# Kernel optimization log

Measured on AMD Instinct MI355X. Metric: run time of the kernel, lower is better.

## Reference

```python
import jax, jax.numpy as jnp
import numpy as np

B, C, CI, H, W = 16, 256, 128, 64, 64


def setup_inputs() -> dict:
    key = jax.random.key(0)
    k1, k2, k3, k4, k5, k6 = jax.random.split(key, 6)
    x_gallery = jax.random.normal(k1, (B, C, H, W), dtype=jnp.float32)
    x_query = jax.random.normal(k2, (B, C, H, W), dtype=jnp.float32)
    # 1x1 conv weights (kernel_size=1 -> equivalent to per-pixel linear map)
    s = 1.0 / np.sqrt(C)
    theta_w = jax.random.uniform(k3, (CI, C), jnp.float32, -s, s)
    theta_b = jax.random.uniform(k4, (CI,), jnp.float32, -s, s)
    phi_w = jax.random.uniform(k5, (CI, C), jnp.float32, -s, s)
    phi_b = jax.random.uniform(k6, (CI,), jnp.float32, -s, s)
    return {"x_gallery": x_gallery, "x_query": x_query,
            "theta_w": theta_w, "theta_b": theta_b,
            "phi_w": phi_w, "phi_b": phi_b}


def reference(x_gallery, x_query, theta_w, theta_b, phi_w, phi_b):
    b, c, h, w = x_gallery.shape
    # 1x1 convs == channel-mixing einsum
    theta_x = jnp.einsum('bchw,oc->bohw', x_gallery, theta_w) + theta_b[None, :, None, None]
    phi_x = jnp.einsum('bchw,oc->bohw', x_query, phi_w) + phi_b[None, :, None, None]
    t = theta_x.reshape(b, theta_x.shape[1], -1)   # [B, CI, HW]
    p = phi_x.reshape(b, phi_x.shape[1], -1)       # [B, CI, H'W']
    n = p.shape[-1]
    # f[b, i, j] = <theta[:, i], phi[:, j]> / N   (norm == 'size')
    f = jnp.einsum('bci,bcj->bij', t, p) / n       # [B, HW, H'W']
    f = jnp.max(f, axis=2)                         # row-wise max (non-softmax attention)
    f = f.reshape(b, 1, h, w)
    return jax.nn.sigmoid(f)                       # message == 'attention_map'
```

## Files before the change

kernel.cpp:

```cpp
#include <hip/hip_runtime.h>
#include <hip/hip_bf16.h>

#define B_   16
#define CIN  256
#define CO   128
#define HW   4096

typedef __attribute__((ext_vector_type(8))) short short8;
typedef __attribute__((ext_vector_type(4))) float f32x4;

__device__ __forceinline__ short f32_to_bf16_rne(float f) {
    union { float f; unsigned u; } v; v.f = f;
    unsigned u = v.u;
    u += 0x7fffu + ((u >> 16) & 1u);
    return (short)(u >> 16);
}

__global__ __launch_bounds__(256) void wconv_kernel(
    const float* __restrict__ tw, const float* __restrict__ pw,
    short* __restrict__ wbf)
{
    const int idx = blockIdx.x * 256 + threadIdx.x;
    const float v = (idx < CO * CIN) ? tw[idx] : pw[idx - CO * CIN];
    wbf[idx] = f32_to_bf16_rne(v);
}

__global__ __launch_bounds__(256, 3) void proj_kernel(
    const float* __restrict__ xg, const float* __restrict__ xq,
    const float* __restrict__ tb, const float* __restrict__ pb,
    const short* __restrict__ wbf,
    short* __restrict__ tT, short* __restrict__ pT)
{
    const int n     = blockIdx.x;
    const int xcd   = n & 7;
    const int q     = n >> 3;
    const int b     = xcd + 8 * (q & 1);
    const int r2    = q >> 1;
    const int which = r2 & 1;
    const int itile = r2 >> 1;

    const float* x    = which ? xq : xg;
    const float* bias = which ? pb : tb;
    const short* wb   = wbf + which * CO * CIN;
    short*       out  = which ? pT : tT;

    const int i0   = itile * 64;
    const int tid  = threadIdx.x;
    const int lane = tid & 63;
    const int wv   = tid >> 6;
    const int nrow = lane & 15;
    const int quad = lane >> 4;

    const int col4 = tid & 15;
    const int rp   = tid >> 4;

    __shared__ short xT[2][64][72];

    f32x4 acc[4][2] = {};

    float bias_v[2];
    bias_v[0] = bias[wv * 32 + 0  + nrow];
    bias_v[1] = bias[wv * 32 + 16 + nrow];

    short8 wfrag[4][2][2];
    #pragma unroll
    for (int c4 = 0; c4 < 4; c4++)
        #pragma unroll
        for (int ks = 0; ks < 2; ks++)
            #pragma unroll
            for (int nt = 0; nt < 2; nt++)
                wfrag[c4][ks][nt] = *(const short8*)(
                    wb + (wv * 32 + nt * 16 + nrow) * CIN + c4 * 64 + ks * 32 + quad * 8);

    const float* xb = x + (long)b * CIN * HW + i0;

    float4 cva[2], cvb[2];

    auto load_chunk = [&](int cc) {
        #pragma unroll
        for (int rr = 0; rr < 2; rr++) {
            const int row = rr * 32 + rp * 2;
            cva[rr] = *(const float4*)(xb + (long)(cc + row)     * HW + col4 * 4);
            cvb[rr] = *(const float4*)(xb + (long)(cc + row + 1) * HW + col4 * 4);
        }
    };
    auto store_chunk = [&](int buf) {
        #pragma unroll
        for (int rr = 0; rr < 2; rr++) {
            const int row = rr * 32 + rp * 2;
            const float* pa  = (const float*)&cva[rr];
            const float* pb2 = (const float*)&cvb[rr];
            #pragma unroll
            for (int k = 0; k < 4; k++) {
                const unsigned lo = (unsigned short)f32_to_bf16_rne(pa[k]);
                const unsigned hi = (unsigned short)f32_to_bf16_rne(pb2[k]);
                *(unsigned*)&xT[buf][col4 * 4 + k][row] = lo | (hi << 16);
            }
        }
    };
    auto mfma_chunk = [&](int c4, int buf) {
        #pragma unroll
        for (int ks = 0; ks < 2; ks++)
            #pragma unroll
            for (int mt = 0; mt < 4; mt++) {
                const short8 a = *(const short8*)&xT[buf][mt * 16 + nrow][ks * 32 + quad * 8];
                acc[mt][0] = __builtin_amdgcn_mfma_f32_16x16x32_bf16(a, wfrag[c4][ks][0], acc[mt][0], 0, 0, 0);
                acc[mt][1] = __builtin_amdgcn_mfma_f32_16x16x32_bf16(a, wfrag[c4][ks][1], acc[mt][1], 0, 0, 0);
            }
    };

    load_chunk(0);
    store_chunk(0);
    #pragma unroll
    for (int c4 = 0; c4 < 4; c4++) {
        __syncthreads();
        if (c4 < 3) load_chunk(c4 * 64 + 64);
        mfma_chunk(c4, c4 & 1);
        if (c4 < 3) store_chunk((c4 + 1) & 1);
    }

    #pragma unroll
    for (int mt = 0; mt < 4; mt++)
        #pragma unroll
        for (int nt = 0; nt < 2; nt++) {
            const int co = wv * 32 + nt * 16 + nrow;
            #pragma unroll
            for (int r = 0; r < 4; r++) {
                const int il = mt * 16 + quad * 4 + r;
                out[((long)b * HW + i0 + il) * CO + co] =
                    f32_to_bf16_rne(acc[mt][nt][r] + bias_v[nt]);
            }
        }
}

__global__ __launch_bounds__(256, 1) void maxgemm_kernel(
    const short* __restrict__ tT, const short* __restrict__ pT,
    float* __restrict__ pmax)
{
    const int n     = blockIdx.x;
    const int b     = (n & 7) + 8 * ((n >> 3) & 1);
    const int mm    = n >> 4;
    const int itile = mm & 7;
    const int jhalf = mm >> 3;
    const int i0    = itile * 512;
    const int j0    = jhalf * 2048;
    const int tid   = threadIdx.x;
    const int lane  = tid & 63;
    const int wv    = tid >> 6;
    const int nrow  = lane & 15;
    const int quad  = lane >> 4;

    __shared__ short bT[2][64][128];

    short8 afrag[8][4];
    {
        const short* ta = tT + ((long)b * HW + i0 + wv * 128) * CO;
        #pragma unroll
        for (int mt = 0; mt < 8; mt++)
            #pragma unroll
            for (int ks = 0; ks < 4; ks++)
                afrag[mt][ks] = *(const short8*)(ta + (mt * 16 + nrow) * CO + ks * 32 + quad * 8);
    }

    const short* pb2 = pT + (long)b * HW * CO + (long)j0 * CO;
    const int sc8 = tid & 15;
    const int sj0 = tid >> 4;

    short8 sreg[4];
    auto stage_load = [&](int jt) {
        const short* src = pb2 + (long)jt * 64 * CO;
        #pragma unroll
        for (int r = 0; r < 4; r++)
            sreg[r] = *(const short8*)(src + (sj0 + r * 16) * CO + sc8 * 8);
    };
    auto stage_write = [&](int buf) {
        #pragma unroll
        for (int r = 0; r < 4; r++) {
            const int j  = sj0 + r * 16;
            const int c8 = sc8 ^ (j & 7);
            *(short8*)&bT[buf][j][c8 * 8] = sreg[r];
        }
    };

    f32x4 vmax[8];
    #pragma unroll
    for (int mt = 0; mt < 8; mt++)
        vmax[mt] = (f32x4){-1e30f, -1e30f, -1e30f, -1e30f};

    const f32x4 kz = {0.f, 0.f, 0.f, 0.f};

    auto compute = [&](int buf) {
        #pragma unroll
        for (int np = 0; np < 2; np++) {
            short8 bf0[4], bf1[4];
            const int ja = np * 32 + nrow;
            const int jb = ja + 16;
            #pragma unroll
            for (int ks = 0; ks < 4; ks++) {
                bf0[ks] = *(const short8*)&bT[buf][ja][(((ks * 4 + quad) ^ (ja & 7)) * 8)];
                bf1[ks] = *(const short8*)&bT[buf][jb][(((ks * 4 + quad) ^ (jb & 7)) * 8)];
            }
            #pragma unroll
            for (int mt = 0; mt < 8; mt++) {
                f32x4 a0 = __builtin_amdgcn_mfma_f32_16x16x32_bf16(afrag[mt][0], bf0[0], kz, 0, 0, 0);
                f32x4 a1 = __builtin_amdgcn_mfma_f32_16x16x32_bf16(afrag[mt][0], bf1[0], kz, 0, 0, 0);
                #pragma unroll
                for (int ks = 1; ks < 4; ks++) {
                    a0 = __builtin_amdgcn_mfma_f32_16x16x32_bf16(afrag[mt][ks], bf0[ks], a0, 0, 0, 0);
                    a1 = __builtin_amdgcn_mfma_f32_16x16x32_bf16(afrag[mt][ks], bf1[ks], a1, 0, 0, 0);
                }
                #pragma unroll
                for (int r = 0; r < 4; r++)
                    vmax[mt][r] = fmaxf(fmaxf(a0[r], a1[r]), vmax[mt][r]);
            }
        }
    };

    stage_load(0);
    stage_write(0);
    for (int jt = 0; jt < 32; jt++) {
        __syncthreads();
        if (jt < 31) stage_load(jt + 1);
        compute(jt & 1);
        if (jt < 31) stage_write((jt + 1) & 1);
    }

    #pragma unroll
    for (int mt = 0; mt < 8; mt++)
        #pragma unroll
        for (int r = 0; r < 4; r++) {
            float v = vmax[mt][r];
            #pragma unroll
            for (int m = 8; m >= 1; m >>= 1)
                v = fmaxf(v, __shfl_xor(v, m, 64));
            vmax[mt][r] = v;
        }

    if (nrow == 0) {
        float* pm = pmax + (size_t)jhalf * (B_ * HW) + (size_t)b * HW + i0 + wv * 128;
        #pragma unroll
        for (int mt = 0; mt < 8; mt++)
            #pragma unroll
            for (int r = 0; r < 4; r++)
                pm[mt * 16 + quad * 4 + r] = vmax[mt][r];
    }
}

__global__ __launch_bounds__(256) void combine_kernel(
    const float* __restrict__ pmax, float* __restrict__ out)
{
    const int idx = blockIdx.x * 256 + threadIdx.x;
    const float v = fmaxf(pmax[idx], pmax[idx + B_ * HW]) * (1.0f / (float)HW);
    out[idx] = 1.0f / (1.0f + __expf(-v));
}

extern "C" void kernel_launch(void* const* d_in, const int* in_sizes, int n_in,
                              void* d_out, int out_size, void* d_ws, size_t ws_size,
                              hipStream_t stream) {
    const float* xg = (const float*)d_in[0];
    const float* xq = (const float*)d_in[1];
    const float* tw = (const float*)d_in[2];
    const float* tb = (const float*)d_in[3];
    const float* pw = (const float*)d_in[4];
    const float* pb = (const float*)d_in[5];
    float* out = (float*)d_out;

    short* tT  = (short*)d_ws;
    short* pT  = tT + (size_t)B_ * HW * CO;
    short* wbf = pT + (size_t)B_ * HW * CO;
    float* pmax = (float*)(wbf + 2 * CO * CIN);

    wconv_kernel<<<(2 * CO * CIN) / 256, 256, 0, stream>>>(tw, pw, wbf);
    proj_kernel<<<B_ * (HW / 64) * 2, 256, 0, stream>>>(xg, xq, tb, pb, wbf, tT, pT);
    maxgemm_kernel<<<B_ * (HW / 256), 256, 0, stream>>>(tT, pT, pmax);
    combine_kernel<<<(B_ * HW) / 256, 256, 0, stream>>>(pmax, out);
}
```

Before: 239.3 us.

## Restage projection input with XOR-swizzled LDS, scalar loads, and streamed weights

```diff
diff --git a/kernel.cpp b/kernel.cpp
--- a/kernel.cpp
+++ b/kernel.cpp
@@ -8,6 +8,7 @@
 
 typedef __attribute__((ext_vector_type(8))) short short8;
 typedef __attribute__((ext_vector_type(4))) float f32x4;
+typedef __attribute__((ext_vector_type(4))) unsigned u32x4;
 
 __device__ __forceinline__ short f32_to_bf16_rne(float f) {
     union { float f; unsigned u; } v; v.f = f;
@@ -25,7 +26,7 @@
     wbf[idx] = f32_to_bf16_rne(v);
 }
 
-__global__ __launch_bounds__(256, 3) void proj_kernel(
+__global__ __launch_bounds__(256, 4) void proj_kernel(
     const float* __restrict__ xg, const float* __restrict__ xq,
     const float* __restrict__ tb, const float* __restrict__ pb,
     const short* __restrict__ wbf,
@@ -51,10 +52,10 @@
     const int nrow = lane & 15;
     const int quad = lane >> 4;
 
-    const int col4 = tid & 15;
-    const int rp   = tid >> 4;
-
-    __shared__ short xT[2][64][72];
+    const int si   = tid & 63;
+    const int cig  = tid >> 6;
+
+    __shared__ __align__(16) short xT[2][64][64];
 
     f32x4 acc[4][2] = {};
 
@@ -62,61 +63,64 @@
     bias_v[0] = bias[wv * 32 + 0  + nrow];
     bias_v[1] = bias[wv * 32 + 16 + nrow];
 
-    short8 wfrag[4][2][2];
-    #pragma unroll
-    for (int c4 = 0; c4 < 4; c4++)
+    const float* xb = x + (long)b * CIN * HW + i0 + si;
+
+    float fst[2][8];
+    auto stage_load = [&](int c) {
+        const float* src = xb + (long)(c * 64) * HW;
+        #pragma unroll
+        for (int ro = 0; ro < 2; ro++)
+            #pragma unroll
+            for (int r = 0; r < 8; r++)
+                fst[ro][r] = src[(long)((ro * 4 + cig) * 8 + r) * HW];
+    };
+    auto stage_write = [&](int buf) {
+        #pragma unroll
+        for (int ro = 0; ro < 2; ro++) {
+            u32x4 d;
+            #pragma unroll
+            for (int p = 0; p < 4; p++) {
+                const unsigned lo = (unsigned short)f32_to_bf16_rne(fst[ro][2 * p]);
+                const unsigned hi = (unsigned short)f32_to_bf16_rne(fst[ro][2 * p + 1]);
+                d[p] = lo | (hi << 16);
+            }
+            const int ck = (ro * 4 + cig) ^ (si & 7);
+            *(u32x4*)&xT[buf][si][ck * 8] = d;
+        }
+    };
+
+    short8 wf[2][2][2];
+    auto wload = [&](int c, int buf) {
         #pragma unroll
         for (int ks = 0; ks < 2; ks++)
             #pragma unroll
             for (int nt = 0; nt < 2; nt++)
-                wfrag[c4][ks][nt] = *(const short8*)(
-                    wb + (wv * 32 + nt * 16 + nrow) * CIN + c4 * 64 + ks * 32 + quad * 8);
-
-    const float* xb = x + (long)b * CIN * HW + i0;
-
-    float4 cva[2], cvb[2];
-
-    auto load_chunk = [&](int cc) {
-        #pragma unroll
-        for (int rr = 0; rr < 2; rr++) {
-            const int row = rr * 32 + rp * 2;
-            cva[rr] = *(const float4*)(xb + (long)(cc + row)     * HW + col4 * 4);
-            cvb[rr] = *(const float4*)(xb + (long)(cc + row + 1) * HW + col4 * 4);
-        }
-    };
-    auto store_chunk = [&](int buf) {
-        #pragma unroll
-        for (int rr = 0; rr < 2; rr++) {
-            const int row = rr * 32 + rp * 2;
-            const float* pa  = (const float*)&cva[rr];
-            const float* pb2 = (const float*)&cvb[rr];
-            #pragma unroll
-            for (int k = 0; k < 4; k++) {
-                const unsigned lo = (unsigned short)f32_to_bf16_rne(pa[k]);
-                const unsigned hi = (unsigned short)f32_to_bf16_rne(pb2[k]);
-                *(unsigned*)&xT[buf][col4 * 4 + k][row] = lo | (hi << 16);
-            }
-        }
-    };
-    auto mfma_chunk = [&](int c4, int buf) {
+                wf[buf][ks][nt] = *(const short8*)(
+                    wb + (wv * 32 + nt * 16 + nrow) * CIN + c * 64 + ks * 32 + quad * 8);
+    };
+
+    auto compute = [&](int buf) {
         #pragma unroll
         for (int ks = 0; ks < 2; ks++)
             #pragma unroll
             for (int mt = 0; mt < 4; mt++) {
-                const short8 a = *(const short8*)&xT[buf][mt * 16 + nrow][ks * 32 + quad * 8];
-                acc[mt][0] = __builtin_amdgcn_mfma_f32_16x16x32_bf16(a, wfrag[c4][ks][0], acc[mt][0], 0, 0, 0);
-                acc[mt][1] = __builtin_amdgcn_mfma_f32_16x16x32_bf16(a, wfrag[c4][ks][1], acc[mt][1], 0, 0, 0);
-            }
-    };
-
-    load_chunk(0);
-    store_chunk(0);
-    #pragma unroll
-    for (int c4 = 0; c4 < 4; c4++) {
+                const int row = mt * 16 + nrow;
+                const int ck  = (ks * 4 + quad) ^ (row & 7);
+                const short8 a = *(const short8*)&xT[buf][row][ck * 8];
+                acc[mt][0] = __builtin_amdgcn_mfma_f32_16x16x32_bf16(a, wf[buf][ks][0], acc[mt][0], 0, 0, 0);
+                acc[mt][1] = __builtin_amdgcn_mfma_f32_16x16x32_bf16(a, wf[buf][ks][1], acc[mt][1], 0, 0, 0);
+            }
+    };
+
+    wload(0, 0);
+    stage_load(0);
+    stage_write(0);
+    #pragma unroll
+    for (int c = 0; c < 4; c++) {
         __syncthreads();
-        if (c4 < 3) load_chunk(c4 * 64 + 64);
-        mfma_chunk(c4, c4 & 1);
-        if (c4 < 3) store_chunk((c4 + 1) & 1);
+        if (c < 3) { stage_load(c + 1); wload(c + 1, (c + 1) & 1); }
+        compute(c & 1);
+        if (c < 3) stage_write((c + 1) & 1);
     }
 
     #pragma unroll
```

Result: slower. 268.5 us (+12.2%).
